# Performance work log

Measured on AMD Instinct MI355X. Metric: run time of the kernel, lower is better.

Reference implementation:

```python
import jax, jax.numpy as jnp
import numpy as np

B, F, H, E, C, K = 32768, 1024, 512, 10, 10, 4  # batch, in_features, hidden, f_enc, num_classes, n_branches


def setup_inputs() -> dict:
    key = jax.random.key(0)
    ks = jax.random.split(key, 12)
    def rn(k, shape, scale):
        return jax.random.normal(k, shape, jnp.float32) * scale
    return {
        "w0": rn(ks[0], (B, F), 1.0),
        "w1": rn(ks[1], (B, F), 1.0),
        "w2": rn(ks[2], (B, F), 1.0),
        "w3": rn(ks[3], (B, F), 1.0),
        # 4 branch linears in -> hidden, stacked on leading axis
        "Wlin": rn(ks[4], (K, H, F), F ** -0.5),
        "blin": jnp.zeros((K, H), jnp.float32),
        # per-branch Q/K/V projections hidden -> f_enc
        "Wq": rn(ks[5], (K, E, H), H ** -0.5),
        "bq": jnp.zeros((K, E), jnp.float32),
        "Wk": rn(ks[6], (K, E, H), H ** -0.5),
        "bk": jnp.zeros((K, E), jnp.float32),
        "Wv": rn(ks[7], (K, E, H), H ** -0.5),
        "bv": jnp.zeros((K, E), jnp.float32),
        # 4 final classifier heads f_enc -> num_classes
        "Wfin": rn(ks[8], (K, C, E), E ** -0.5),
        "bfin": jnp.zeros((K, C), jnp.float32),
    }


def reference(w0, w1, w2, w3, Wlin, blin, Wq, bq, Wk, bk, Wv, bv, Wfin, bfin):
    # dropout is identity in eval mode
    w = jnp.stack([w0, w1, w2, w3], axis=1)              # [B,K,F]
    h = jnp.einsum('bkf,khf->bkh', w, Wlin) + blin        # [B,K,H]
    q = jnp.einsum('bkh,keh->bke', h, Wq) + bq            # [B,K,E]
    k_enc = jnp.einsum('bkh,keh->bke', h, Wk) + bk        # [B,K,E]
    v = jnp.einsum('bkh,keh->bke', h, Wv) + bv            # [B,K,E]
    # einsum 'bij,bil->bjl' contracts the branch axis (i == K)
    attn = jnp.einsum('bke,bkl->bel', q, k_enc) / np.float32(np.sqrt(E))  # [B,E,E]
    attn = jax.nn.softmax(attn, axis=1)                   # torch Softmax(dim=1)
    att_out = jnp.einsum('bnm,bkm->bkn', attn, v)         # [B,K,E]
    w0o = att_out[:, 0, :]                                # original uses index 0 for all four heads
    logits = jnp.einsum('be,kce->bkc', w0o, Wfin) + bfin  # [B,K,C]
    outputs = jnp.mean(jax.nn.softmax(logits, axis=-1), axis=1)  # 0.25 * sum of 4 softmaxed heads
    return (outputs, attn)
```

## Files before the change

kernel.cpp:

```cpp
#include <hip/hip_runtime.h>
#include <stdint.h>

#define B_ROWS 32768
#define F_DIM  1024
#define H_DIM  512

typedef __attribute__((ext_vector_type(4))) float    floatx4;
typedef __attribute__((ext_vector_type(2))) __fp16   fp16x2;
typedef __attribute__((ext_vector_type(8))) _Float16 halfx8;

__device__ __forceinline__ void async_load16(const void* g, void* l) {
    __builtin_amdgcn_global_load_lds(
        (const __attribute__((address_space(1))) void*)g,
        (__attribute__((address_space(3))) void*)l, 16, 0, 0);
}

__global__ __launch_bounds__(256) void k_prep(
    const float* __restrict__ Wlin, const float* __restrict__ blin,
    const float* __restrict__ Wq, const float* __restrict__ Wk,
    const float* __restrict__ Wv, const float* __restrict__ bq,
    const float* __restrict__ bk, const float* __restrict__ bv,
    ushort* __restrict__ Wcomb16, float* __restrict__ bcomb)
{
    const int k = blockIdx.x >> 5;
    const int d = blockIdx.x & 31;
    const int t = threadIdx.x;
    ushort4* outp = (ushort4*)(Wcomb16 + ((size_t)(k * 32 + d) << 10)) + t;

    if (d >= 30) {
        ushort4 z; z.x = z.y = z.z = z.w = 0;
        *outp = z;
        if (t == 0) bcomb[k * 32 + d] = 0.f;
        return;
    }

    const float* wrow; float bias;
    if (d < 10)      { wrow = Wq + (size_t)(k * 10 + d) * H_DIM;      bias = bq[k * 10 + d]; }
    else if (d < 20) { wrow = Wk + (size_t)(k * 10 + d - 10) * H_DIM; bias = bk[k * 10 + d - 10]; }
    else             { wrow = Wv + (size_t)(k * 10 + d - 20) * H_DIM; bias = bv[k * 10 + d - 20]; }

    const float* wl = Wlin + ((size_t)k * H_DIM << 10) + t * 4;
    const float* bl = blin + (size_t)k * H_DIM;

    floatx4 acc = {0.f, 0.f, 0.f, 0.f};
    float bacc = 0.f;
    #pragma unroll 4
    for (int h = 0; h < H_DIM; ++h) {
        const float s = wrow[h];
        const floatx4 x = *(const floatx4*)(wl + ((size_t)h << 10));
        acc.x += s * x.x; acc.y += s * x.y; acc.z += s * x.z; acc.w += s * x.w;
        bacc += s * bl[h];
    }
    union { _Float16 h[4]; ushort4 u; } o;
    o.h[0] = (_Float16)acc.x; o.h[1] = (_Float16)acc.y;
    o.h[2] = (_Float16)acc.z; o.h[3] = (_Float16)acc.w;
    *outp = o.u;
    if (t == 0) bcomb[k * 32 + d] = bias + bacc;
}

__global__ __launch_bounds__(256) void k_main(
    const float* __restrict__ w0, const float* __restrict__ w1,
    const float* __restrict__ w2, const float* __restrict__ w3,
    const ushort* __restrict__ Wcomb16, const float* __restrict__ bcomb,
    float* __restrict__ qkv_t)
{
    __shared__ float  As[128 * 64];
    __shared__ ushort Bs[32 * 64];

    const int tid     = threadIdx.x;
    const int bx      = blockIdx.x;
    const int k       = bx & 3;
    const int rowBase = (bx >> 2) * 128;

    const float* A = (k == 0) ? w0 : (k == 1) ? w1 : (k == 2) ? w2 : w3;

    const int arow  = tid >> 4;
    const int ascol = ((tid & 15) ^ (arow & 7)) * 4;
    const int brow  = tid >> 3;
    const int bscol = ((tid & 7) ^ (brow & 7)) * 8;

    const float*  gA0 = A + (size_t)(rowBase + arow) * F_DIM + ascol;
    const ushort* gB0 = Wcomb16 + (size_t)(k * 32 + brow) * 1024 + bscol;
    float*  lA = &As[tid * 4];
    ushort* lB = &Bs[tid * 8];

    const int wv = tid >> 6;
    const int ln = tid & 63;
    const int lr = ln & 15;
    const int lq = ln >> 4;
    const int sw = lr & 7;

    floatx4 acc[2][2] = {};

    for (int kc = 0; kc < F_DIM; kc += 64) {
        __syncthreads();
        #pragma unroll
        for (int it = 0; it < 8; ++it)
            async_load16(gA0 + kc + it * 16 * F_DIM, lA + it * 16 * 64);
        async_load16(gB0 + kc, lB);
        __syncthreads();

        #pragma unroll
        for (int ks = 0; ks < 2; ++ks) {
            halfx8 af[2];
            #pragma unroll
            for (int i = 0; i < 2; ++i) {
                const int rbase = (wv * 32 + i * 16 + lr) * 64;
                const int s0 = (ks * 8 + lq * 2) ^ sw;
                const floatx4 f0 = *(const floatx4*)&As[rbase + s0 * 4];
                const floatx4 f1 = *(const floatx4*)&As[rbase + (s0 ^ 1) * 4];
                union { fp16x2 h2[4]; halfx8 h8; } u;
                u.h2[0] = __builtin_amdgcn_cvt_pkrtz(f0.x, f0.y);
                u.h2[1] = __builtin_amdgcn_cvt_pkrtz(f0.z, f0.w);
                u.h2[2] = __builtin_amdgcn_cvt_pkrtz(f1.x, f1.y);
                u.h2[3] = __builtin_amdgcn_cvt_pkrtz(f1.z, f1.w);
                af[i] = u.h8;
            }
            #pragma unroll
            for (int j = 0; j < 2; ++j) {
                const int bs = (ks * 4 + lq) ^ sw;
                const halfx8 bf = *(const halfx8*)&Bs[(j * 16 + lr) * 64 + bs * 8];
                acc[0][j] = __builtin_amdgcn_mfma_f32_16x16x32_f16(af[0], bf, acc[0][j], 0, 0, 0);
                acc[1][j] = __builtin_amdgcn_mfma_f32_16x16x32_f16(af[1], bf, acc[1][j], 0, 0, 0);
            }
        }
    }

    const float* bc = bcomb + k * 32;
    #pragma unroll
    for (int j = 0; j < 2; ++j) {
        const int d = j * 16 + lr;
        if (d < 30) {
            const float bias = bc[d];
            float* outd = qkv_t + (size_t)(k * 30 + d) * B_ROWS;
            #pragma unroll
            for (int i = 0; i < 2; ++i) {
                const int r0 = rowBase + wv * 32 + i * 16 + lq * 4;
                floatx4 o = acc[i][j];
                o.x += bias; o.y += bias; o.z += bias; o.w += bias;
                *(floatx4*)(outd + r0) = o;
            }
        }
    }
}

__global__ __launch_bounds__(128) void k_final(
    const float* __restrict__ qkv_t, const float* __restrict__ Wfin,
    const float* __restrict__ bfin,
    float* __restrict__ outputs, float* __restrict__ attn)
{
    __shared__ float sW[400];
    __shared__ float sb[40];
    const int t = threadIdx.x;
    for (int i = t; i < 400; i += 128) sW[i] = Wfin[i];
    if (t < 40) sb[t] = bfin[t];
    __syncthreads();

    const int b = blockIdx.x * 128 + t;
    const float* pt = qkv_t + b;
    float q[4][10], kk[4][10], v0[10];
    #pragma unroll
    for (int k = 0; k < 4; ++k)
        #pragma unroll
        for (int e = 0; e < 10; ++e) {
            q[k][e]  = pt[(size_t)(k * 30 + e) * B_ROWS];
            kk[k][e] = pt[(size_t)(k * 30 + 10 + e) * B_ROWS];
        }
    #pragma unroll
    for (int m = 0; m < 10; ++m) v0[m] = pt[(size_t)(20 + m) * B_ROWS];

    float out0[10];
    #pragma unroll
    for (int e = 0; e < 10; ++e) out0[e] = 0.f;
    float* ab = attn + (size_t)b * 100;
    const float inv = 0.31622776601683794f;

    #pragma unroll
    for (int m = 0; m < 10; ++m) {
        float col[10]; float mx = -1e30f;
        #pragma unroll
        for (int e = 0; e < 10; ++e) {
            col[e] = (q[0][e]*kk[0][m] + q[1][e]*kk[1][m]
                    + q[2][e]*kk[2][m] + q[3][e]*kk[3][m]) * inv;
            mx = fmaxf(mx, col[e]);
        }
        float s = 0.f;
        #pragma unroll
        for (int e = 0; e < 10; ++e) { col[e] = __expf(col[e] - mx); s += col[e]; }
        const float r = 1.f / s;
        #pragma unroll
        for (int e = 0; e < 10; ++e) {
            const float a = col[e] * r;
            ab[e * 10 + m] = a;
            out0[e] += a * v0[m];
        }
    }

    float oc[10];
    #pragma unroll
    for (int c = 0; c < 10; ++c) oc[c] = 0.f;
    #pragma unroll
    for (int k = 0; k < 4; ++k) {
        float lg[10]; float mx = -1e30f;
        #pragma unroll
        for (int c = 0; c < 10; ++c) {
            float s = sb[k * 10 + c];
            #pragma unroll
            for (int e = 0; e < 10; ++e) s += out0[e] * sW[(k * 10 + c) * 10 + e];
            lg[c] = s; mx = fmaxf(mx, s);
        }
        float s = 0.f;
        #pragma unroll
        for (int c = 0; c < 10; ++c) { lg[c] = __expf(lg[c] - mx); s += lg[c]; }
        const float r = 0.25f / s;
        #pragma unroll
        for (int c = 0; c < 10; ++c) oc[c] += lg[c] * r;
    }
    #pragma unroll
    for (int c = 0; c < 10; ++c) outputs[(size_t)b * 10 + c] = oc[c];
}

extern "C" void kernel_launch(void* const* d_in, const int* in_sizes, int n_in,
                              void* d_out, int out_size, void* d_ws, size_t ws_size,
                              hipStream_t stream) {
    const float* w0   = (const float*)d_in[0];
    const float* w1   = (const float*)d_in[1];
    const float* w2   = (const float*)d_in[2];
    const float* w3   = (const float*)d_in[3];
    const float* Wlin = (const float*)d_in[4];
    const float* blin = (const float*)d_in[5];
    const float* Wq   = (const float*)d_in[6];
    const float* bq   = (const float*)d_in[7];
    const float* Wk   = (const float*)d_in[8];
    const float* bk   = (const float*)d_in[9];
    const float* Wv   = (const float*)d_in[10];
    const float* bv   = (const float*)d_in[11];
    const float* Wfin = (const float*)d_in[12];
    const float* bfin = (const float*)d_in[13];

    char* ws = (char*)d_ws;
    ushort* Wcomb16 = (ushort*)ws;
    float*  bcomb   = (float*)(ws + ((size_t)256 << 10));
    float*  qkv_t   = (float*)(ws + ((size_t)1 << 20));

    float* outputs = (float*)d_out;
    float* attn    = outputs + (size_t)B_ROWS * 10;

    k_prep <<<128,  256, 0, stream>>>(Wlin, blin, Wq, Wk, Wv, bq, bk, bv, Wcomb16, bcomb);
    k_main <<<1024, 256, 0, stream>>>(w0, w1, w2, w3, Wcomb16, bcomb, qkv_t);
    k_final<<<256,  128, 0, stream>>>(qkv_t, Wfin, bfin, outputs, attn);
}
```

Before: 576.9 us.

## Double-buffer main GEMM loads, coalesce final-kernel stores, split prep blocks, pad qkv stride

```diff
diff --git a/kernel.cpp b/kernel.cpp
--- a/kernel.cpp
+++ b/kernel.cpp
@@ -4,6 +4,7 @@
 #define B_ROWS 32768
 #define F_DIM  1024
 #define H_DIM  512
+#define RS     32832
 
 typedef __attribute__((ext_vector_type(4))) float    floatx4;
 typedef __attribute__((ext_vector_type(2))) __fp16   fp16x2;
@@ -15,22 +16,25 @@
         (__attribute__((address_space(3))) void*)l, 16, 0, 0);
 }
 
-__global__ __launch_bounds__(256) void k_prep(
+__global__ __launch_bounds__(128) void k_prep(
     const float* __restrict__ Wlin, const float* __restrict__ blin,
     const float* __restrict__ Wq, const float* __restrict__ Wk,
     const float* __restrict__ Wv, const float* __restrict__ bq,
     const float* __restrict__ bk, const float* __restrict__ bv,
     ushort* __restrict__ Wcomb16, float* __restrict__ bcomb)
 {
-    const int k = blockIdx.x >> 5;
-    const int d = blockIdx.x & 31;
-    const int t = threadIdx.x;
-    ushort4* outp = (ushort4*)(Wcomb16 + ((size_t)(k * 32 + d) << 10)) + t;
+    const int bx   = blockIdx.x;
+    const int k    = bx >> 6;
+    const int d    = (bx >> 1) & 31;
+    const int half = bx & 1;
+    const int t    = threadIdx.x;
+    const int col  = half * 512 + t * 4;
+    ushort4* outp = (ushort4*)(Wcomb16 + ((size_t)(k * 32 + d) << 10) + col);
 
     if (d >= 30) {
         ushort4 z; z.x = z.y = z.z = z.w = 0;
         *outp = z;
-        if (t == 0) bcomb[k * 32 + d] = 0.f;
+        if (half == 0 && t == 0) bcomb[k * 32 + d] = 0.f;
         return;
     }
 
@@ -39,12 +43,12 @@
     else if (d < 20) { wrow = Wk + (size_t)(k * 10 + d - 10) * H_DIM; bias = bk[k * 10 + d - 10]; }
     else             { wrow = Wv + (size_t)(k * 10 + d - 20) * H_DIM; bias = bv[k * 10 + d - 20]; }
 
-    const float* wl = Wlin + ((size_t)k * H_DIM << 10) + t * 4;
+    const float* wl = Wlin + ((size_t)k * H_DIM << 10) + col;
     const float* bl = blin + (size_t)k * H_DIM;
 
     floatx4 acc = {0.f, 0.f, 0.f, 0.f};
     float bacc = 0.f;
-    #pragma unroll 4
+    #pragma unroll 8
     for (int h = 0; h < H_DIM; ++h) {
         const float s = wrow[h];
         const floatx4 x = *(const floatx4*)(wl + ((size_t)h << 10));
@@ -55,7 +59,7 @@
     o.h[0] = (_Float16)acc.x; o.h[1] = (_Float16)acc.y;
     o.h[2] = (_Float16)acc.z; o.h[3] = (_Float16)acc.w;
     *outp = o.u;
-    if (t == 0) bcomb[k * 32 + d] = bias + bacc;
+    if (half == 0 && t == 0) bcomb[k * 32 + d] = bias + bacc;
 }
 
 __global__ __launch_bounds__(256) void k_main(
@@ -64,8 +68,8 @@
     const ushort* __restrict__ Wcomb16, const float* __restrict__ bcomb,
     float* __restrict__ qkv_t)
 {
-    __shared__ float  As[128 * 64];
-    __shared__ ushort Bs[32 * 64];
+    __shared__ float  As[2][128 * 64];
+    __shared__ ushort Bs[2][32 * 64];
 
     const int tid     = threadIdx.x;
     const int bx      = blockIdx.x;
@@ -81,8 +85,6 @@
 
     const float*  gA0 = A + (size_t)(rowBase + arow) * F_DIM + ascol;
     const ushort* gB0 = Wcomb16 + (size_t)(k * 32 + brow) * 1024 + bscol;
-    float*  lA = &As[tid * 4];
-    ushort* lB = &Bs[tid * 8];
 
     const int wv = tid >> 6;
     const int ln = tid & 63;
@@ -92,13 +94,29 @@
 
     floatx4 acc[2][2] = {};
 
-    for (int kc = 0; kc < F_DIM; kc += 64) {
-        __syncthreads();
-        #pragma unroll
-        for (int it = 0; it < 8; ++it)
-            async_load16(gA0 + kc + it * 16 * F_DIM, lA + it * 16 * 64);
-        async_load16(gB0 + kc, lB);
-        __syncthreads();
+    #define STAGE(buf, kc) do {                                            \
+        float*  lAb = &As[buf][tid * 4];                                   \
+        ushort* lBb = &Bs[buf][tid * 8];                                   \
+        _Pragma("unroll")                                                  \
+        for (int it = 0; it < 8; ++it)                                     \
+            async_load16(gA0 + (kc) + it * 16 * F_DIM, lAb + it * 16 * 64);\
+        async_load16(gB0 + (kc), lBb);                                     \
+    } while (0)
+
+    STAGE(0, 0);
+
+    #pragma unroll 2
+    for (int t = 0; t < 16; ++t) {
+        const int cur = t & 1;
+        if (t < 15) {
+            STAGE(cur ^ 1, (t + 1) * 64);
+            asm volatile("s_waitcnt vmcnt(9)" ::: "memory");
+        } else {
+            asm volatile("s_waitcnt vmcnt(0)" ::: "memory");
+        }
+        __builtin_amdgcn_sched_barrier(0);
+        __builtin_amdgcn_s_barrier();
+        __builtin_amdgcn_sched_barrier(0);
 
         #pragma unroll
         for (int ks = 0; ks < 2; ++ks) {
@@ -107,8 +125,8 @@
             for (int i = 0; i < 2; ++i) {
                 const int rbase = (wv * 32 + i * 16 + lr) * 64;
                 const int s0 = (ks * 8 + lq * 2) ^ sw;
-                const floatx4 f0 = *(const floatx4*)&As[rbase + s0 * 4];
-                const floatx4 f1 = *(const floatx4*)&As[rbase + (s0 ^ 1) * 4];
+                const floatx4 f0 = *(const floatx4*)&As[cur][rbase + s0 * 4];
+                const floatx4 f1 = *(const floatx4*)&As[cur][rbase + (s0 ^ 1) * 4];
                 union { fp16x2 h2[4]; halfx8 h8; } u;
                 u.h2[0] = __builtin_amdgcn_cvt_pkrtz(f0.x, f0.y);
                 u.h2[1] = __builtin_amdgcn_cvt_pkrtz(f0.z, f0.w);
@@ -119,12 +137,15 @@
             #pragma unroll
             for (int j = 0; j < 2; ++j) {
                 const int bs = (ks * 4 + lq) ^ sw;
-                const halfx8 bf = *(const halfx8*)&Bs[(j * 16 + lr) * 64 + bs * 8];
+                const halfx8 bf = *(const halfx8*)&Bs[cur][(j * 16 + lr) * 64 + bs * 8];
                 acc[0][j] = __builtin_amdgcn_mfma_f32_16x16x32_f16(af[0], bf, acc[0][j], 0, 0, 0);
                 acc[1][j] = __builtin_amdgcn_mfma_f32_16x16x32_f16(af[1], bf, acc[1][j], 0, 0, 0);
             }
         }
-    }
+        __builtin_amdgcn_sched_barrier(0);
+        __builtin_amdgcn_s_barrier();
+    }
+    #undef STAGE
 
     const float* bc = bcomb + k * 32;
     #pragma unroll
@@ -132,7 +153,7 @@
         const int d = j * 16 + lr;
         if (d < 30) {
             const float bias = bc[d];
-            float* outd = qkv_t + (size_t)(k * 30 + d) * B_ROWS;
+            float* outd = qkv_t + (size_t)(k * 30 + d) * RS;
             #pragma unroll
             for (int i = 0; i < 2; ++i) {
                 const int r0 = rowBase + wv * 32 + i * 16 + lq * 4;
@@ -151,6 +172,7 @@
 {
     __shared__ float sW[400];
     __shared__ float sb[40];
+    __shared__ float sA[128 * 101];
     const int t = threadIdx.x;
     for (int i = t; i < 400; i += 128) sW[i] = Wfin[i];
     if (t < 40) sb[t] = bfin[t];
@@ -163,16 +185,16 @@
     for (int k = 0; k < 4; ++k)
         #pragma unroll
         for (int e = 0; e < 10; ++e) {
-            q[k][e]  = pt[(size_t)(k * 30 + e) * B_ROWS];
-            kk[k][e] = pt[(size_t)(k * 30 + 10 + e) * B_ROWS];
-        }
-    #pragma unroll
-    for (int m = 0; m < 10; ++m) v0[m] = pt[(size_t)(20 + m) * B_ROWS];
+            q[k][e]  = pt[(size_t)(k * 30 + e) * RS];
+            kk[k][e] = pt[(size_t)(k * 30 + 10 + e) * RS];
+        }
+    #pragma unroll
+    for (int m = 0; m < 10; ++m) v0[m] = pt[(size_t)(20 + m) * RS];
 
     float out0[10];
     #pragma unroll
     for (int e = 0; e < 10; ++e) out0[e] = 0.f;
-    float* ab = attn + (size_t)b * 100;
+    float* sAr = &sA[t * 101];
     const float inv = 0.31622776601683794f;
 
     #pragma unroll
@@ -191,7 +213,7 @@
         #pragma unroll
         for (int e = 0; e < 10; ++e) {
             const float a = col[e] * r;
-            ab[e * 10 + m] = a;
+            sAr[e * 10 + m] = a;
             out0[e] += a * v0[m];
         }
     }
@@ -216,8 +238,23 @@
         #pragma unroll
         for (int c = 0; c < 10; ++c) oc[c] += lg[c] * r;
     }
-    #pragma unroll
-    for (int c = 0; c < 10; ++c) outputs[(size_t)b * 10 + c] = oc[c];
+
+    __syncthreads();
+    const size_t abase = (size_t)blockIdx.x * 12800;
+    for (int i = t; i < 12800; i += 128) {
+        const int bl = i / 100;
+        attn[abase + i] = sA[bl * 101 + (i - bl * 100)];
+    }
+
+    __syncthreads();
+    #pragma unroll
+    for (int c = 0; c < 10; ++c) sA[t * 11 + c] = oc[c];
+    __syncthreads();
+    const size_t obase = (size_t)blockIdx.x * 1280;
+    for (int i = t; i < 1280; i += 128) {
+        const int bl = i / 10;
+        outputs[obase + i] = sA[bl * 11 + (i - bl * 10)];
+    }
 }
 
 extern "C" void kernel_launch(void* const* d_in, const int* in_sizes, int n_in,
@@ -246,7 +283,7 @@
     float* outputs = (float*)d_out;
     float* attn    = outputs + (size_t)B_ROWS * 10;
 
-    k_prep <<<128,  256, 0, stream>>>(Wlin, blin, Wq, Wk, Wv, bq, bk, bv, Wcomb16, bcomb);
+    k_prep <<<256,  128, 0, stream>>>(Wlin, blin, Wq, Wk, Wv, bq, bk, bv, Wcomb16, bcomb);
     k_main <<<1024, 256, 0, stream>>>(w0, w1, w2, w3, Wcomb16, bcomb, qkv_t);
     k_final<<<256,  128, 0, stream>>>(qkv_t, Wfin, bfin, outputs, attn);
 }
```

After: 518.4 us. -10.1%, faster.
